# Performance work log

Measured on AMD Instinct MI355X. Metric: run time of the kernel, lower is better.

Reference implementation:

```python
import jax, jax.numpy as jnp
import numpy as np

D = 128
HIDDEN = 512
N = 2048


def setup_inputs() -> dict:
    key = jax.random.key(0)
    k_x, k0, k1, k2 = jax.random.split(key, 4)
    x = jax.random.normal(k_x, (N, D), dtype=jnp.float32)
    # LocallyConnected init: uniform(-sqrt(1/in), sqrt(1/in))
    b0 = 1.0 / np.sqrt(D)
    b1 = 1.0 / np.sqrt(HIDDEN)
    W0 = jax.random.uniform(k0, (D, D, HIDDEN), jnp.float32, -b0, b0)
    W1 = jax.random.uniform(k1, (D, HIDDEN, HIDDEN), jnp.float32, -b1, b1)
    W2 = jax.random.uniform(k2, (D, HIDDEN, 1), jnp.float32, -b1, b1)
    return {"x": x, "W0": W0, "W1": W1, "W2": W2}


def reference(x, W0, W1, W2):
    n, d = x.shape
    # masking layer: matmul with diag(mask[i]) == elementwise zero-out of diagonal
    mask = 1.0 - jnp.eye(d, dtype=x.dtype)          # [d, d]
    h = x[:, None, :] * mask[None, :, :]            # [n, d, d]
    # per-node locally-connected MLP
    h = jax.nn.leaky_relu(jnp.einsum('ndi,dio->ndo', h, W0))   # [n, d, hidden]
    h = jax.nn.leaky_relu(jnp.einsum('ndi,dio->ndo', h, W1))   # [n, d, hidden]
    h = jnp.einsum('ndi,dio->ndo', h, W2)                      # [n, d, 1]
    return h.squeeze(-1)                                       # [n, d]
```

## Files before the change

kernel.cpp:

```cpp
#include <hip/hip_runtime.h>

#define DD 128
#define HH 512
#define NN 2048
#define NT 64
#define PLD 516

typedef __bf16 bf16x8 __attribute__((ext_vector_type(8)));
typedef __bf16 bf16x4 __attribute__((ext_vector_type(4)));
typedef float  floatx4  __attribute__((ext_vector_type(4)));
typedef float  floatx16 __attribute__((ext_vector_type(16)));

typedef const __attribute__((address_space(1))) void* as1cv;
typedef __attribute__((address_space(3))) void* as3v;

__global__ void cvt_x(const float* __restrict__ x, __bf16* __restrict__ xb) {
    int t = blockIdx.x * blockDim.x + threadIdx.x;
    float4 v = *(const float4*)(x + (size_t)t * 4);
    bf16x4 o;
    o[0] = (__bf16)v.x; o[1] = (__bf16)v.y; o[2] = (__bf16)v.z; o[3] = (__bf16)v.w;
    *(bf16x4*)(xb + (size_t)t * 4) = o;
}

__global__ void pack_w(const float* __restrict__ W, __bf16* __restrict__ Wp, int nks32) {
    __shared__ __bf16 Ls[32 * PLD];
    const int d  = blockIdx.x / nks32;
    const int ks = blockIdx.x % nks32;
    const int tid = threadIdx.x;
    const int nks16 = nks32 * 2;
    const float* src = W + ((size_t)(d * nks32 + ks) * 32) * HH;

#pragma unroll
    for (int it = 0; it < 16; ++it) {
        int e = (it * 256 + tid) * 4;
        float4 v = *(const float4*)(src + e);
        bf16x4 o;
        o[0] = (__bf16)v.x; o[1] = (__bf16)v.y; o[2] = (__bf16)v.z; o[3] = (__bf16)v.w;
        *(bf16x4*)(Ls + (e >> 9) * PLD + (e & 511)) = o;
    }
    __syncthreads();

#pragma unroll
    for (int it = 0; it < 8; ++it) {
        int u  = it * 256 + tid;
        int l  = u & 63;
        int ct = (u >> 6) & 15;
        int kh = u >> 10;
        int lr = l & 31, lh = l >> 5;
        bf16x8 v;
#pragma unroll
        for (int j = 0; j < 8; ++j)
            v[j] = Ls[(kh * 16 + lh * 8 + j) * PLD + ct * 32 + lr];
        *(bf16x8*)(Wp + ((size_t)(d * 16 + ct) * nks16 + (ks * 2 + kh)) * 512 + l * 8) = v;
    }
}

__launch_bounds__(512, 4)
__global__ void grandag_main(const __bf16* __restrict__ xb,
                             const __bf16* __restrict__ W0p,
                             const __bf16* __restrict__ W1p,
                             const float* __restrict__ W2,
                             float* __restrict__ out) {
    __shared__ __bf16 h1s[NT * HH];
    __shared__ float  outp2[8][NT];
    __shared__ float  w2s[HH];

    const int b  = blockIdx.x;
    const int d  = ((b >> 8) << 3) | (b & 7);
    const int n0 = ((b >> 3) & 31) * NT;

    const int tid = threadIdx.x;
    const int wq  = __builtin_amdgcn_readfirstlane(tid >> 6);
    const int l   = tid & 63;
    const int lr  = l & 31;
    const int lh  = l >> 5;
    const int swz = lr & 7;

    const int kz  = d >> 4;
    const int lhz = (d >> 3) & 1;
    const int jz  = d & 7;

    if (wq < 2) {
        const float* g = W2 + (size_t)d * HH + (size_t)(wq * 64 + l) * 4;
        __builtin_amdgcn_global_load_lds((as1cv)g, (as3v)(w2s + wq * 256), 16, 0, 0);
    }

    {
        floatx16 acc[2][2] = {};
        const __bf16* W0b = W0p + ((size_t)(d * 16 + wq * 2) * 8) * 512 + (size_t)l * 8;
        const __bf16* xbb = xb + (size_t)(n0 + lr) * DD + lh * 8;

        int ke = wq & 7;
        bf16x8 wa0 = *(const bf16x8*)(W0b + (size_t)ke * 512);
        bf16x8 wa1 = *(const bf16x8*)(W0b + (size_t)(8 + ke) * 512);
#pragma unroll
        for (int i = 0; i < 8; i++) {
            const int kn = (ke + 1) & 7;
            bf16x8 wb0 = *(const bf16x8*)(W0b + (size_t)kn * 512);
            bf16x8 wb1 = *(const bf16x8*)(W0b + (size_t)(8 + kn) * 512);
            bf16x8 x0 = *(const bf16x8*)(xbb + (size_t)ke * 16);
            bf16x8 x1 = *(const bf16x8*)(xbb + (size_t)(32 * DD) + ke * 16);
            if (ke == kz && lh == lhz) {
#pragma unroll
                for (int j = 0; j < 8; j++)
                    if (j == jz) { x0[j] = (__bf16)0.f; x1[j] = (__bf16)0.f; }
            }
            acc[0][0] = __builtin_amdgcn_mfma_f32_32x32x16_bf16(wa0, x0, acc[0][0], 0, 0, 0);
            acc[0][1] = __builtin_amdgcn_mfma_f32_32x32x16_bf16(wa0, x1, acc[0][1], 0, 0, 0);
            acc[1][0] = __builtin_amdgcn_mfma_f32_32x32x16_bf16(wa1, x0, acc[1][0], 0, 0, 0);
            acc[1][1] = __builtin_amdgcn_mfma_f32_32x32x16_bf16(wa1, x1, acc[1][1], 0, 0, 0);
            wa0 = wb0; wa1 = wb1; ke = kn;
        }
#pragma unroll
        for (int mt = 0; mt < 2; mt++) {
#pragma unroll
            for (int q2 = 0; q2 < 4; q2++) {
                const int chunk = 8 * wq + 4 * mt + q2;
#pragma unroll
                for (int nt = 0; nt < 2; nt++) {
                    const int row = nt * 32 + lr;
                    bf16x4 o;
#pragma unroll
                    for (int i = 0; i < 4; i++) {
                        float v = acc[mt][nt][q2 * 4 + i];
                        o[i] = (__bf16)fmaxf(v, 0.01f * v);
                    }
                    *(bf16x4*)(h1s + (size_t)row * HH + ((chunk ^ swz) << 3) + 4 * lh) = o;
                }
            }
        }
    }
    __syncthreads();

    floatx16 acc2[2][2] = {};
    {
        const __bf16* W1b  = W1p + ((size_t)(d * 16 + wq * 2) * 32) * 512 + (size_t)l * 8;
        const __bf16* h1b0 = h1s + (size_t)lr * HH;
        const __bf16* h1b1 = h1s + (size_t)(32 + lr) * HH;

        int ke = (wq * 4) & 31;
        bf16x8 wa0 = *(const bf16x8*)(W1b + (size_t)ke * 512);
        bf16x8 wa1 = *(const bf16x8*)(W1b + (size_t)(32 + ke) * 512);
#pragma unroll
        for (int i = 0; i < 32; i++) {
            const int kn = (ke + 1) & 31;
            bf16x8 wb0 = *(const bf16x8*)(W1b + (size_t)kn * 512);
            bf16x8 wb1 = *(const bf16x8*)(W1b + (size_t)(32 + kn) * 512);
            const int hoff = ((2 * ke + lh) ^ swz) << 3;
            bf16x8 h0  = *(const bf16x8*)(h1b0 + hoff);
            bf16x8 h1v = *(const bf16x8*)(h1b1 + hoff);
            acc2[0][0] = __builtin_amdgcn_mfma_f32_32x32x16_bf16(wa0, h0,  acc2[0][0], 0, 0, 0);
            acc2[0][1] = __builtin_amdgcn_mfma_f32_32x32x16_bf16(wa0, h1v, acc2[0][1], 0, 0, 0);
            acc2[1][0] = __builtin_amdgcn_mfma_f32_32x32x16_bf16(wa1, h0,  acc2[1][0], 0, 0, 0);
            acc2[1][1] = __builtin_amdgcn_mfma_f32_32x32x16_bf16(wa1, h1v, acc2[1][1], 0, 0, 0);
            wa0 = wb0; wa1 = wb1; ke = kn;
        }
    }

    {
        const float* W2b = w2s + wq * 64 + lh * 4;
#pragma unroll
        for (int nt = 0; nt < 2; nt++) {
            float s = 0.f;
#pragma unroll
            for (int mt = 0; mt < 2; mt++) {
#pragma unroll
                for (int q2 = 0; q2 < 4; q2++) {
                    floatx4 w2q = *(const floatx4*)(W2b + mt * 32 + 8 * q2);
#pragma unroll
                    for (int i = 0; i < 4; i++) {
                        float v = acc2[mt][nt][q2 * 4 + i];
                        s += fmaxf(v, 0.01f * v) * w2q[i];
                    }
                }
            }
            s += __shfl_xor(s, 32, 64);
            if (!lh) outp2[wq][nt * 32 + lr] = s;
        }
    }
    __syncthreads();
    if (tid < NT) {
        float v = 0.f;
#pragma unroll
        for (int ww = 0; ww < 8; ww++) v += outp2[ww][tid];
        out[(size_t)(n0 + tid) * DD + d] = v;
    }
}

extern "C" void kernel_launch(void* const* d_in, const int* in_sizes, int n_in,
                              void* d_out, int out_size, void* d_ws, size_t ws_size,
                              hipStream_t stream) {
    const float* x  = (const float*)d_in[0];
    const float* W0 = (const float*)d_in[1];
    const float* W1 = (const float*)d_in[2];
    const float* W2 = (const float*)d_in[3];
    float* out = (float*)d_out;

    __bf16* W0p = (__bf16*)d_ws;
    __bf16* W1p = (__bf16*)((char*)d_ws + (size_t)DD * DD * HH * 2);
    __bf16* xb  = (__bf16*)((char*)d_ws + (size_t)DD * DD * HH * 2
                                        + (size_t)DD * HH * HH * 2);

    cvt_x<<<dim3(NN * DD / (256 * 4)), 256, 0, stream>>>(x, xb);
    pack_w<<<dim3(DD * (DD / 32)), 256, 0, stream>>>(W0, W0p, DD / 32);
    pack_w<<<dim3(DD * (HH / 32)), 256, 0, stream>>>(W1, W1p, HH / 32);

    grandag_main<<<dim3(DD * (NN / NT)), 512, 0, stream>>>(xb, W0p, W1p, W2, out);
}
```

Measured before the change: 418.7 us.

## Deepen weight prefetch pipelines and replace LDS swizzle with padded rows

The layer-0 and layer-1 MFMA loops now prefetch weights two and four k-steps ahead through register ring buffers instead of one. The per-wave rotated k start is dropped, so all waves walk k from zero. The XOR swizzle on the h1 LDS tile is replaced by a padded row stride of 520, and the next h1 fragment is loaded one iteration early. Launch bounds drop from 4 to 3 blocks per CU to leave room for the extra registers. The aim is to hide global-load latency, at the cost of lower occupancy and possibly more bank or cache contention now that waves share the same k order.

```diff
diff --git a/kernel.cpp b/kernel.cpp
--- a/kernel.cpp
+++ b/kernel.cpp
@@ -5,6 +5,7 @@
 #define NN 2048
 #define NT 64
 #define PLD 516
+#define PLD2 520
 
 typedef __bf16 bf16x8 __attribute__((ext_vector_type(8)));
 typedef __bf16 bf16x4 __attribute__((ext_vector_type(4)));
@@ -55,13 +56,13 @@
     }
 }
 
-__launch_bounds__(512, 4)
+__launch_bounds__(512, 3)
 __global__ void grandag_main(const __bf16* __restrict__ xb,
                              const __bf16* __restrict__ W0p,
                              const __bf16* __restrict__ W1p,
                              const float* __restrict__ W2,
                              float* __restrict__ out) {
-    __shared__ __bf16 h1s[NT * HH];
+    __shared__ __bf16 h1s[NT * PLD2];
     __shared__ float  outp2[8][NT];
     __shared__ float  w2s[HH];
 
@@ -74,7 +75,6 @@
     const int l   = tid & 63;
     const int lr  = l & 31;
     const int lh  = l >> 5;
-    const int swz = lr & 7;
 
     const int kz  = d >> 4;
     const int lhz = (d >> 3) & 1;
@@ -90,26 +90,31 @@
         const __bf16* W0b = W0p + ((size_t)(d * 16 + wq * 2) * 8) * 512 + (size_t)l * 8;
         const __bf16* xbb = xb + (size_t)(n0 + lr) * DD + lh * 8;
 
-        int ke = wq & 7;
-        bf16x8 wa0 = *(const bf16x8*)(W0b + (size_t)ke * 512);
-        bf16x8 wa1 = *(const bf16x8*)(W0b + (size_t)(8 + ke) * 512);
-#pragma unroll
-        for (int i = 0; i < 8; i++) {
-            const int kn = (ke + 1) & 7;
-            bf16x8 wb0 = *(const bf16x8*)(W0b + (size_t)kn * 512);
-            bf16x8 wb1 = *(const bf16x8*)(W0b + (size_t)(8 + kn) * 512);
-            bf16x8 x0 = *(const bf16x8*)(xbb + (size_t)ke * 16);
-            bf16x8 x1 = *(const bf16x8*)(xbb + (size_t)(32 * DD) + ke * 16);
-            if (ke == kz && lh == lhz) {
+        bf16x8 wbuf[2][2];
+#pragma unroll
+        for (int s = 0; s < 2; s++) {
+            wbuf[s][0] = *(const bf16x8*)(W0b + (size_t)s * 512);
+            wbuf[s][1] = *(const bf16x8*)(W0b + (size_t)(8 + s) * 512);
+        }
+#pragma unroll
+        for (int ks = 0; ks < 8; ks++) {
+            const int s = ks & 1;
+            bf16x8 w0 = wbuf[s][0], w1 = wbuf[s][1];
+            if (ks + 2 < 8) {
+                wbuf[s][0] = *(const bf16x8*)(W0b + (size_t)(ks + 2) * 512);
+                wbuf[s][1] = *(const bf16x8*)(W0b + (size_t)(8 + ks + 2) * 512);
+            }
+            bf16x8 x0 = *(const bf16x8*)(xbb + (size_t)ks * 16);
+            bf16x8 x1 = *(const bf16x8*)(xbb + (size_t)(32 * DD) + ks * 16);
+            if (ks == kz && lh == lhz) {
 #pragma unroll
                 for (int j = 0; j < 8; j++)
                     if (j == jz) { x0[j] = (__bf16)0.f; x1[j] = (__bf16)0.f; }
             }
-            acc[0][0] = __builtin_amdgcn_mfma_f32_32x32x16_bf16(wa0, x0, acc[0][0], 0, 0, 0);
-            acc[0][1] = __builtin_amdgcn_mfma_f32_32x32x16_bf16(wa0, x1, acc[0][1], 0, 0, 0);
-            acc[1][0] = __builtin_amdgcn_mfma_f32_32x32x16_bf16(wa1, x0, acc[1][0], 0, 0, 0);
-            acc[1][1] = __builtin_amdgcn_mfma_f32_32x32x16_bf16(wa1, x1, acc[1][1], 0, 0, 0);
-            wa0 = wb0; wa1 = wb1; ke = kn;
+            acc[0][0] = __builtin_amdgcn_mfma_f32_32x32x16_bf16(w0, x0, acc[0][0], 0, 0, 0);
+            acc[0][1] = __builtin_amdgcn_mfma_f32_32x32x16_bf16(w0, x1, acc[0][1], 0, 0, 0);
+            acc[1][0] = __builtin_amdgcn_mfma_f32_32x32x16_bf16(w1, x0, acc[1][0], 0, 0, 0);
+            acc[1][1] = __builtin_amdgcn_mfma_f32_32x32x16_bf16(w1, x1, acc[1][1], 0, 0, 0);
         }
 #pragma unroll
         for (int mt = 0; mt < 2; mt++) {
@@ -125,7 +130,7 @@
                         float v = acc[mt][nt][q2 * 4 + i];
                         o[i] = (__bf16)fmaxf(v, 0.01f * v);
                     }
-                    *(bf16x4*)(h1s + (size_t)row * HH + ((chunk ^ swz) << 3) + 4 * lh) = o;
+                    *(bf16x4*)(h1s + (size_t)row * PLD2 + chunk * 8 + lh * 4) = o;
                 }
             }
         }
@@ -135,25 +140,34 @@
     floatx16 acc2[2][2] = {};
     {
         const __bf16* W1b  = W1p + ((size_t)(d * 16 + wq * 2) * 32) * 512 + (size_t)l * 8;
-        const __bf16* h1b0 = h1s + (size_t)lr * HH;
-        const __bf16* h1b1 = h1s + (size_t)(32 + lr) * HH;
-
-        int ke = (wq * 4) & 31;
-        bf16x8 wa0 = *(const bf16x8*)(W1b + (size_t)ke * 512);
-        bf16x8 wa1 = *(const bf16x8*)(W1b + (size_t)(32 + ke) * 512);
+        const __bf16* h1b0 = h1s + (size_t)lr * PLD2;
+        const __bf16* h1b1 = h1s + (size_t)(32 + lr) * PLD2;
+
+        bf16x8 wbuf[4][2];
+#pragma unroll
+        for (int s = 0; s < 4; s++) {
+            wbuf[s][0] = *(const bf16x8*)(W1b + (size_t)s * 512);
+            wbuf[s][1] = *(const bf16x8*)(W1b + (size_t)(32 + s) * 512);
+        }
+        bf16x8 h0  = *(const bf16x8*)(h1b0 + lh * 8);
+        bf16x8 h1v = *(const bf16x8*)(h1b1 + lh * 8);
 #pragma unroll
         for (int i = 0; i < 32; i++) {
-            const int kn = (ke + 1) & 31;
-            bf16x8 wb0 = *(const bf16x8*)(W1b + (size_t)kn * 512);
-            bf16x8 wb1 = *(const bf16x8*)(W1b + (size_t)(32 + kn) * 512);
-            const int hoff = ((2 * ke + lh) ^ swz) << 3;
-            bf16x8 h0  = *(const bf16x8*)(h1b0 + hoff);
-            bf16x8 h1v = *(const bf16x8*)(h1b1 + hoff);
-            acc2[0][0] = __builtin_amdgcn_mfma_f32_32x32x16_bf16(wa0, h0,  acc2[0][0], 0, 0, 0);
-            acc2[0][1] = __builtin_amdgcn_mfma_f32_32x32x16_bf16(wa0, h1v, acc2[0][1], 0, 0, 0);
-            acc2[1][0] = __builtin_amdgcn_mfma_f32_32x32x16_bf16(wa1, h0,  acc2[1][0], 0, 0, 0);
-            acc2[1][1] = __builtin_amdgcn_mfma_f32_32x32x16_bf16(wa1, h1v, acc2[1][1], 0, 0, 0);
-            wa0 = wb0; wa1 = wb1; ke = kn;
+            const int s = i & 3;
+            bf16x8 w0 = wbuf[s][0], w1 = wbuf[s][1];
+            if (i + 4 < 32) {
+                wbuf[s][0] = *(const bf16x8*)(W1b + (size_t)(i + 4) * 512);
+                wbuf[s][1] = *(const bf16x8*)(W1b + (size_t)(32 + i + 4) * 512);
+            }
+            bf16x8 hc0 = h0, hc1 = h1v;
+            if (i + 1 < 32) {
+                h0  = *(const bf16x8*)(h1b0 + (2 * (i + 1) + lh) * 8);
+                h1v = *(const bf16x8*)(h1b1 + (2 * (i + 1) + lh) * 8);
+            }
+            acc2[0][0] = __builtin_amdgcn_mfma_f32_32x32x16_bf16(w0, hc0, acc2[0][0], 0, 0, 0);
+            acc2[0][1] = __builtin_amdgcn_mfma_f32_32x32x16_bf16(w0, hc1, acc2[0][1], 0, 0, 0);
+            acc2[1][0] = __builtin_amdgcn_mfma_f32_32x32x16_bf16(w1, hc0, acc2[1][0], 0, 0, 0);
+            acc2[1][1] = __builtin_amdgcn_mfma_f32_32x32x16_bf16(w1, hc1, acc2[1][1], 0, 0, 0);
         }
     }
 
```

Result: slower. 478.7 us (+14.3%).
